# Performance work log

Measured on AMD Instinct MI355X. Metric: run time of the kernel, lower is better.

Reference implementation:

```python
import jax, jax.numpy as jnp
import numpy as np

S, N, LAT, HID, NH, NLAYERS = 8, 128, 128, 384, 8, 6
HT, WT, DT = 128, 128, 128
DIN, DOUT, RAD, LEVELS, FED = 1169, 3 + 3 * 128, 3, 4, 64


def sincos1d(d, pos):
    # MAE-style 1d sincos embedding, d even -> [..., d]
    omega = 1.0 / (10000.0 ** (jnp.arange(d // 2, dtype=jnp.float32) / (d / 2.0)))
    ang = pos[..., None] * omega
    return jnp.concatenate([jnp.sin(ang), jnp.cos(ang)], axis=-1)


def flow_embed(f, Cd=FED):
    # get_3d_embedding(flows, 64, cat_coords=True) -> [..., 3*Cd+3] = 195
    div = jnp.arange(0, Cd, 2, dtype=jnp.float32) * (1000.0 / Cd)
    outs = []
    for a in range(3):
        ang = f[..., a, None] * div
        pe = jnp.stack([jnp.sin(ang), jnp.cos(ang)], axis=-1).reshape(f.shape[:-1] + (Cd,))
        outs.append(pe)
    return jnp.concatenate(outs + [f], axis=-1)


def avg_pool2(x):
    B, Sv, Cc, H, W = x.shape
    return x.reshape(B, Sv, Cc, H // 2, 2, W // 2, 2).mean(axis=(4, 6))


def pyramid(fm):
    pyr = [fm]
    for _ in range(LEVELS - 1):
        fm = avg_pool2(fm)
        pyr.append(fm)
    return pyr


def bilinear_sample(corr, xy):
    # corr: [B,S,N,H,W]; xy: [B,S,N,P,2] pixel coords (x indexes W, y indexes H); zero padding
    B, Sv, Nn, H, W = corr.shape
    cf = corr.reshape(B, Sv, Nn, H * W)
    x, y = xy[..., 0], xy[..., 1]
    x0f = jnp.floor(x); y0f = jnp.floor(y)
    wx, wy = x - x0f, y - y0f
    x0 = x0f.astype(jnp.int32); y0 = y0f.astype(jnp.int32)

    def gather(xi, yi):
        ok = ((xi >= 0) & (xi < W) & (yi >= 0) & (yi < H)).astype(cf.dtype)
        idx = jnp.clip(yi, 0, H - 1) * W + jnp.clip(xi, 0, W - 1)
        v = jnp.take_along_axis(cf, idx.reshape(B, Sv, Nn, -1), axis=-1).reshape(idx.shape)
        return v * ok

    v00 = gather(x0, y0); v01 = gather(x0 + 1, y0)
    v10 = gather(x0, y0 + 1); v11 = gather(x0 + 1, y0 + 1)
    return v00 * (1 - wx) * (1 - wy) + v01 * wx * (1 - wy) + v10 * (1 - wx) * wy + v11 * wx * wy


def corr_sample(pyr, targets, coords):
    # RAFT/CoTracker CorrBlock: per-level dense correlation then (2r+1)^2 window bilinear lookup
    d = jnp.arange(-RAD, RAD + 1, dtype=jnp.float32)
    delta = jnp.stack(jnp.meshgrid(d, d, indexing="ij"), axis=-1).reshape(-1, 2)  # [49,2]
    scale = 1.0 / jnp.sqrt(jnp.float32(targets.shape[-1]))
    outs = []
    for l, fm in enumerate(pyr):
        corr = jnp.einsum("bsnc,bschw->bsnhw", targets, fm) * scale
        xy = coords[..., None, :] / (2.0 ** l) + delta
        outs.append(bilinear_sample(corr, xy))
    return jnp.concatenate(outs, axis=-1)  # [B,S,N,196]


def layernorm(x, g, b):
    m = x.mean(-1, keepdims=True)
    v = x.var(-1, keepdims=True)
    return (x - m) / jnp.sqrt(v + 1e-5) * g + b


def attention(x, Wqkv, bq, Wo, bo):
    M, T, H = x.shape
    dh = H // NH
    qkv = (x @ Wqkv + bq).reshape(M, T, 3, NH, dh)
    q, k, v = qkv[:, :, 0], qkv[:, :, 1], qkv[:, :, 2]
    att = jax.nn.softmax(jnp.einsum("mthd,mshd->mhts", q, k) / jnp.sqrt(jnp.float32(dh)), axis=-1)
    o = jnp.einsum("mhts,mshd->mthd", att, v).reshape(M, T, H)
    return o @ Wo + bo


def updateformer(x, support, W_in, b_in, lnp, Wqkv, bqkv, Wo, bo, W1, b1, W2, b2, W_out, b_out, Ws, bs):
    # x: [B,N,T,DIN]; alternating time (over T) and space (over N) pre-LN transformer blocks
    B, Np, T, _ = x.shape
    sproj = support @ Ws + bs  # [100,HID]
    h = x @ W_in + b_in + sproj.mean(axis=0)
    for i in range(NLAYERS):
        g1, bb1, g2, bb2 = lnp[i, 0], lnp[i, 1], lnp[i, 2], lnp[i, 3]
        if i % 2 == 0:
            y = h.reshape(B * Np, T, HID)
        else:
            y = h.transpose(0, 2, 1, 3).reshape(B * T, Np, HID)
        y = y + attention(layernorm(y, g1, bb1), Wqkv[i], bqkv[i], Wo[i], bo[i])
        z = layernorm(y, g2, bb2)
        y = y + jax.nn.gelu(z @ W1[i] + b1[i], approximate=False) @ W2[i] + b2[i]
        if i % 2 == 0:
            h = y.reshape(B, Np, T, HID)
        else:
            h = y.reshape(B, T, Np, HID).transpose(0, 2, 1, 3)
    return h @ W_out + b_out, sproj[None]


def groupnorm1(x, g, b):
    m = x.mean(-1, keepdims=True)
    v = x.var(-1, keepdims=True)
    return (x - m) / jnp.sqrt(v + 1e-5) * g + b


def _forward(fmapXY, fmapYZ, fmapXZ, coords_init, vis_init, track_mask, feat_init, support_features,
             W_in, b_in, lnp, Wqkv, bqkv, Wo, bo, W1, b1, W2, b2, W_out, b_out, Ws, bs,
             gn_g, gn_b, Wu, bu, Wvis, bvis, iters):
    B, Sv, Cc, H, W = fmapXY.shape
    D = fmapXZ.shape[-2]
    Nn = coords_init.shape[2]
    coords = coords_init
    ffeats = [feat_init[..., k] for k in range(3)]
    pyrXY, pyrYZ, pyrXZ = pyramid(fmapXY), pyramid(fmapYZ), pyramid(fmapXZ)
    grid_size = jnp.array([H, W, D], dtype=jnp.float32)
    # 3d sincos pos embed from query coords; 1169 padded to 1170 -> 390/axis, truncated back
    g = (coords[:, 0] / grid_size * 2.0 - 1.0) * 128.0  # [B,N,3]
    pe = jnp.concatenate([sincos1d(390, g[..., i]) for i in range(3)], axis=-1)[..., :DIN]
    pos_embed = pe.reshape(B * Nn, 1, DIN)
    times_embed = sincos1d(1170, jnp.arange(Sv, dtype=jnp.float32))[None, :, :DIN]
    support = support_features
    for _ in range(iters):
        coords = jax.lax.stop_gradient(coords)  # matches coords.detach()
        fxy = corr_sample(pyrXY, ffeats[0], coords[..., :2])
        fyz = corr_sample(pyrYZ, ffeats[1], coords[..., 1:3])
        fxz = corr_sample(pyrXZ, ffeats[2], coords[..., 0::2])
        fcorrs = jnp.concatenate([fxy, fyz, fxz], axis=-1)  # [B,S,N,588]
        fcorrs_ = fcorrs.transpose(0, 2, 1, 3).reshape(B * Nn, Sv, -1)
        flows_ = (coords - coords[:, :1]).transpose(0, 2, 1, 3).reshape(B * Nn, Sv, 3)
        flows_cat = flow_embed(flows_)  # [BN,S,195]
        ff = [f.transpose(0, 2, 1, 3).reshape(B * Nn, Sv, LAT) for f in ffeats]
        ffeats_ = jnp.concatenate(ff, axis=-1)  # [BN,S,384]
        # replicate torch's cat(dim=2)+permute+reshape layout exactly
        tmv = jnp.concatenate([track_mask, vis_init], axis=2).transpose(0, 2, 1, 3).reshape(B * Nn, Sv, 2)
        tin = jnp.concatenate([flows_cat, fcorrs_, ffeats_, tmv], axis=-1)  # [BN,S,1169]
        x = (tin + pos_embed + times_embed).reshape(B, Nn, Sv, DIN)
        delta, dse3 = updateformer(x, support, W_in, b_in, lnp, Wqkv, bqkv, Wo, bo, W1, b1, W2, b2, W_out, b_out, Ws, bs)
        support = support + dse3[0] / 100.0
        delta = delta.reshape(B * Nn, Sv, DOUT)
        d_coord = delta[..., :3].reshape(B, Nn, Sv, 3).transpose(0, 2, 1, 3)
        coords = coords + d_coord
        new_ffeats = []
        for k in range(3):
            dfk = delta[..., 3 + k * LAT:3 + (k + 1) * LAT]
            upd = jax.nn.gelu(groupnorm1(dfk, gn_g[k], gn_b[k]) @ Wu[k] + bu[k], approximate=False)
            new_ffeats.append(ffeats[k] + upd.reshape(B, Nn, Sv, LAT).transpose(0, 2, 1, 3))
        ffeats = new_ffeats
    vis = (jnp.concatenate(ffeats, axis=-1) @ Wvis + bvis)[..., 0]  # [B,S,N]
    return jnp.concatenate([coords, vis[..., None]], axis=-1)  # [B,S,N,4]


def setup_inputs() -> dict:
    key = jax.random.key(0)
    ks = jax.random.split(key, 16)
    f32 = jnp.float32
    B = 1
    fmapXY = jax.random.normal(ks[0], (B, S, LAT, HT, WT), f32)
    fmapYZ = jax.random.normal(ks[1], (B, S, LAT, DT, HT), f32)
    fmapXZ = jax.random.normal(ks[2], (B, S, LAT, DT, WT), f32)
    coords_init = jax.random.uniform(ks[3], (B, S, N, 3), f32) * 112.0 + 8.0
    vis_init = jnp.ones((B, S, N, 1), f32)
    track_mask = jnp.ones((B, S, N, 1), f32)
    feat_init = jax.random.normal(ks[4], (B, S, N, LAT, 3), f32)
    support_features = jnp.zeros((100, HID), f32) + 0.1
    w = lambda k, sh: jax.random.normal(k, sh, f32) * 0.02
    ln1 = jnp.stack([jnp.ones(HID, f32), jnp.zeros(HID, f32), jnp.ones(HID, f32), jnp.zeros(HID, f32)])
    params = dict(
        W_in=w(ks[5], (DIN, HID)), b_in=jnp.zeros((HID,), f32),
        lnp=jnp.tile(ln1[None], (NLAYERS, 1, 1)),
        Wqkv=w(ks[6], (NLAYERS, HID, 3 * HID)), bqkv=jnp.zeros((NLAYERS, 3 * HID), f32),
        Wo=w(ks[7], (NLAYERS, HID, HID)), bo=jnp.zeros((NLAYERS, HID), f32),
        W1=w(ks[8], (NLAYERS, HID, 4 * HID)), b1=jnp.zeros((NLAYERS, 4 * HID), f32),
        W2=w(ks[9], (NLAYERS, 4 * HID, HID)), b2=jnp.zeros((NLAYERS, HID), f32),
        W_out=w(ks[10], (HID, DOUT)), b_out=jnp.zeros((DOUT,), f32),
        Ws=w(ks[11], (HID, HID)), bs=jnp.zeros((HID,), f32),
        gn_g=jnp.ones((3, LAT), f32), gn_b=jnp.zeros((3, LAT), f32),
        Wu=w(ks[12], (3, LAT, LAT)), bu=jnp.zeros((3, LAT), f32),
        Wvis=w(ks[13], (3 * LAT, 1)), bvis=jnp.zeros((1,), f32),
    )
    return dict(fmapXY=fmapXY, fmapYZ=fmapYZ, fmapXZ=fmapXZ, coords_init=coords_init,
                vis_init=vis_init, track_mask=track_mask, feat_init=feat_init,
                support_features=support_features, iters=2, **params)


def reference(fmapXY, fmapYZ, fmapXZ, coords_init, vis_init, track_mask, feat_init, support_features,
              W_in, b_in, lnp, Wqkv, bqkv, Wo, bo, W1, b1, W2, b2, W_out, b_out, Ws, bs,
              gn_g, gn_b, Wu, bu, Wvis, bvis, iters):
    return _forward(fmapXY, fmapYZ, fmapXZ, coords_init, vis_init, track_mask, feat_init, support_features,
                    W_in, b_in, lnp, Wqkv, bqkv, Wo, bo, W1, b1, W2, b2, W_out, b_out, Ws, bs,
                    gn_g, gn_b, Wu, bu, Wvis, bvis, iters)
```

## Files before the change

kernel.cpp:

```cpp
#include <hip/hip_runtime.h>
#include <hip/hip_bf16.h>


#define DEVFN __device__ __forceinline__

typedef __attribute__((ext_vector_type(8))) short short8;
typedef __attribute__((ext_vector_type(4))) float f32x4;

static constexpr float INV_SQRT_DH = 0.14433756729740643f;
static constexpr float CORR_SCALE  = 0.08838834764831845f;
static constexpr size_t VSTRIDE = 22282240;

DEVFN float gelu_exact(float x){
  return 0.5f * x * (1.0f + erff(x * 0.7071067811865476f));
}
DEVFN short bf16_of(float f){
  __hip_bfloat16 b = __float2bfloat16(f);
  return *reinterpret_cast<short*>(&b);
}
DEVFN float bfu(uint32_t u16){ return __uint_as_float(u16 << 16); }
DEVFN float bf2f(__hip_bfloat16 b){ return __bfloat162float(b); }

DEVFN f32x4 MFMA(short8 a, short8 b, f32x4 c){
  return __builtin_amdgcn_mfma_f32_16x16x32_bf16(a,b,c,0,0,0);
}

template<int K, int MODE, bool AF32, int DEPTH>
static __device__ void mgemm_body(int bx, int by, const void* __restrict__ A, int lda,
                                  const __hip_bfloat16* __restrict__ Bt,
                                  float* __restrict__ C, int ldc,
                                  int M, int N, const float* __restrict__ bias, int tid){
  constexpr int NSTEP = K/32;
  int lane = tid & 63, wid = tid >> 6;
  int wr = wid >> 1, wc = wid & 1;
  int lr = lane & 15, lk = lane >> 4;
  int m0 = by*64 + wr*32;
  int n0 = bx*64 + wc*32;

  const __hip_bfloat16* Ab = (const __hip_bfloat16*)A;
  const float* Af = (const float*)A;
  size_t arow0 = (size_t)(m0 + lr)      * lda;
  size_t arow1 = (size_t)(m0 + 16 + lr) * lda;
  size_t brow0 = (size_t)(n0 + lr)      * K;
  size_t brow1 = (size_t)(n0 + 16 + lr) * K;

  auto loadA = [&](size_t ro, int k0)->short8{
    if constexpr (AF32){
      const float* p = Af + ro + k0 + lk*8;
      short8 r;
      #pragma unroll
      for (int j=0;j<8;j++) r[j] = bf16_of(p[j]);
      return r;
    } else {
      return *reinterpret_cast<const short8*>(Ab + ro + k0 + lk*8);
    }
  };
  auto loadB = [&](size_t ro, int k0)->short8{
    return *reinterpret_cast<const short8*>(Bt + ro + k0 + lk*8);
  };

  short8 a0[DEPTH], a1[DEPTH], b0[DEPTH], b1[DEPTH];
  #pragma unroll
  for (int p=0;p<DEPTH;p++){
    if (p < NSTEP){
      a0[p]=loadA(arow0,p*32); a1[p]=loadA(arow1,p*32);
      b0[p]=loadB(brow0,p*32); b1[p]=loadB(brow1,p*32);
    }
  }
  f32x4 acc00 = {}, acc01 = {}, acc10 = {}, acc11 = {};
  #pragma unroll
  for (int t=0;t<NSTEP;t++){
    const int cur = t % DEPTH;
    acc00 = MFMA(a0[cur],b0[cur],acc00);
    acc01 = MFMA(a0[cur],b1[cur],acc01);
    acc10 = MFMA(a1[cur],b0[cur],acc10);
    acc11 = MFMA(a1[cur],b1[cur],acc11);
    if (t+DEPTH < NSTEP){
      int k0 = (t+DEPTH)*32;
      a0[cur]=loadA(arow0,k0); a1[cur]=loadA(arow1,k0);
      b0[cur]=loadB(brow0,k0); b1[cur]=loadB(brow1,k0);
    }
  }

  f32x4 accs[2][2] = {{acc00, acc01},{acc10, acc11}};
  #pragma unroll
  for (int mi=0;mi<2;mi++){
    #pragma unroll
    for (int ni=0;ni<2;ni++){
      int c = n0 + ni*16 + lr;
      if (c >= N) continue;
      float bv = bias ? bias[c] : 0.0f;
      #pragma unroll
      for (int reg=0;reg<4;reg++){
        int r = m0 + mi*16 + lk*4 + reg;
        if (r >= M) continue;
        float v = accs[mi][ni][reg] + bv;
        if (MODE==0) C[(size_t)r*ldc + c] = v;
        else C[(size_t)r*ldc + c] += v;
      }
    }
  }
}

__global__ void transpose_init_k(const float* __restrict__ inXY, const float* __restrict__ inYZ,
                                 const float* __restrict__ inXZ, __hip_bfloat16* __restrict__ pyr,
                                 float* coords, const float* cinit,
                                 float* ff, const float* feat_init,
                                 float* support, const float* sfeat,
                                 float* posE, float* timE){
  int bid = blockIdx.x;
  int tid = threadIdx.x;
  if (bid >= 12288){
    int idx = (bid - 12288)*256 + tid;
    if (idx < 3072)  coords[idx]  = cinit[idx];
    if (idx < 49152){
      int row = idx / 384;
      support[idx] = (row < 100) ? sfeat[idx] : 0.0f;
    }
    if (idx < 393216){
      int k = idx / 131072, rest = idx % 131072;
      ff[idx] = feat_init[(size_t)rest*3 + k];
    }
    if (idx < 149632){
      int n = idx / 1169, d = idx % 1169;
      int i = d / 390, dd = d % 390;
      float c = cinit[n*3 + i];
      float g = (c / 128.0f * 2.0f - 1.0f) * 128.0f;
      int m = (dd < 195) ? dd : dd - 195;
      float om = powf(10000.0f, -(float)m / 195.0f);
      float ang = g * om;
      posE[idx] = (dd < 195) ? sinf(ang) : cosf(ang);
    }
    if (idx < 9352){
      int s = idx / 1169, d = idx % 1169;
      int m = (d < 585) ? d : d - 585;
      float om = powf(10000.0f, -(float)m / 585.0f);
      float ang = (float)s * om;
      timE[idx] = (d < 585) ? sinf(ang) : cosf(ang);
    }
    return;
  }
  __shared__ float tile[128][33];
  int vz = bid >> 9;
  int v = vz >> 3, s = vz & 7;
  const float* in = (v==0) ? inXY : ((v==1) ? inYZ : inXZ);
  int h0 = (bid & 511) * 32;
  const float* ib = in + (size_t)s*128*16384;
  int chunk = tid & 7;
  int cbase = tid >> 3;
  #pragma unroll
  for (int r=0;r<4;r++){
    int c = cbase + r*32;
    float4 f = *reinterpret_cast<const float4*>(ib + (size_t)c*16384 + h0 + chunk*4);
    tile[c][chunk*4+0]=f.x; tile[c][chunk*4+1]=f.y;
    tile[c][chunk*4+2]=f.z; tile[c][chunk*4+3]=f.w;
  }
  __syncthreads();
  __hip_bfloat16* ob = pyr + (size_t)v*VSTRIDE + (size_t)s*16384*128;
  int w = tid >> 6, lane = tid & 63;
  #pragma unroll
  for (int rr=0;rr<8;rr++){
    int hw = w*8 + rr;
    uint32_t lo = (uint32_t)(uint16_t)bf16_of(tile[2*lane][hw]);
    uint32_t hi = (uint32_t)(uint16_t)bf16_of(tile[2*lane+1][hw]);
    reinterpret_cast<uint32_t*>(ob + (size_t)(h0+hw)*128)[lane] = lo | (hi<<16);
  }
}

__global__ void pool2_k(__hip_bfloat16* __restrict__ pyr, size_t in_off, size_t out_off, int So){
  int idx = blockIdx.x*256 + threadIdx.x;
  int total = 8*So*So*128;
  if (idx >= total) return;
  const __hip_bfloat16* in = pyr + (size_t)blockIdx.z*VSTRIDE + in_off;
  __hip_bfloat16* out      = pyr + (size_t)blockIdx.z*VSTRIDE + out_off;
  int c = idx & 127;
  int x = (idx >> 7) % So;
  int y = ((idx >> 7) / So) % So;
  int s = idx / (So*So*128);
  int Si = So*2;
  const __hip_bfloat16* b0 = in + (((size_t)s*Si + 2*y)*Si + 2*x)*128 + c;
  float v = bf2f(b0[0]) + bf2f(b0[128])
          + bf2f(b0[(size_t)Si*128]) + bf2f(b0[(size_t)Si*128 + 128]);
  out[idx] = __float2bfloat16(v*0.25f);
}

__global__ void wtrans_all_k(const float* Ws, const float* W_in, const float* Wqkv,
                             const float* Wo, const float* W1, const float* W2,
                             const float* W_out, const float* Wu,
                             __hip_bfloat16* WsT, __hip_bfloat16* WinT, __hip_bfloat16* WqkvT,
                             __hip_bfloat16* WoT, __hip_bfloat16* W1T, __hip_bfloat16* W2T,
                             __hip_bfloat16* WoutT, __hip_bfloat16* WuT){
  __shared__ float tile[32][33];
  int z = blockIdx.z;
  const float* in; __hip_bfloat16* out; int K,N,Kp,Np;
  if (z==0){ in=Ws; out=WsT; K=384;N=384;Kp=384;Np=384; }
  else if (z==1){ in=W_in; out=WinT; K=1169;N=384;Kp=1184;Np=384; }
  else if (z<8){ int l=z-2; in=Wqkv+(size_t)l*442368; out=WqkvT+(size_t)l*442368; K=384;N=1152;Kp=384;Np=1152; }
  else if (z<14){ int l=z-8; in=Wo+(size_t)l*147456; out=WoT+(size_t)l*147456; K=384;N=384;Kp=384;Np=384; }
  else if (z<20){ int l=z-14; in=W1+(size_t)l*589824; out=W1T+(size_t)l*589824; K=384;N=1536;Kp=384;Np=1536; }
  else if (z<26){ int l=z-20; in=W2+(size_t)l*589824; out=W2T+(size_t)l*589824; K=1536;N=384;Kp=1536;Np=384; }
  else if (z==26){ in=W_out; out=WoutT; K=384;N=387;Kp=384;Np=448; }
  else { int l=z-27; in=Wu+(size_t)l*16384; out=WuT+(size_t)l*16384; K=128;N=128;Kp=128;Np=128; }
  int MK = (K>Kp)?K:Kp, MN = (N>Np)?N:Np;
  int kb = blockIdx.y*32, nb = blockIdx.x*32;
  if (kb >= MK || nb >= MN) return;
  int tx = threadIdx.x & 31, ty = threadIdx.x >> 5;
  #pragma unroll
  for (int r=0;r<4;r++){
    int k = kb + ty + r*8, n = nb + tx;
    tile[ty+r*8][tx] = (k < K && n < N) ? in[(size_t)k*N + n] : 0.0f;
  }
  __syncthreads();
  #pragma unroll
  for (int r=0;r<4;r++){
    int n = nb + ty + r*8, k = kb + tx;
    if (n < Np && k < Kp) out[(size_t)n*Kp + k] = __float2bfloat16(tile[tx][ty+r*8]);
  }
}

__global__ void assemble_x_k(__hip_bfloat16* __restrict__ xbuf, const float* __restrict__ posE,
                             const float* __restrict__ timE, const float* __restrict__ coords,
                             const float* __restrict__ ff, const float* __restrict__ tmask,
                             const float* __restrict__ vinit,
                             const float* __restrict__ support,
                             const __hip_bfloat16* __restrict__ WsT,
                             float* __restrict__ sproj, const float* __restrict__ bs){
  if (blockIdx.x >= 1024){
    int b = blockIdx.x - 1024;
    mgemm_body<384,0,true,3>(b%6, b/6, support,384, WsT, sproj,384, 100,384, bs, threadIdx.x);
    return;
  }
  int r = blockIdx.x;
  int n = r >> 3, s = r & 7;
  for (int d = threadIdx.x; d < 1184; d += blockDim.x){
    __hip_bfloat16* dst = xbuf + (size_t)r*1184 + d;
    if (d >= 1169){ *dst = __float2bfloat16(0.0f); continue; }
    float base = posE[(size_t)n*1169 + d] + timE[(size_t)s*1169 + d];
    if (d >= 195 && d < 783){ *dst = __float2bfloat16(base); continue; }
    float val;
    if (d < 195){
      if (d >= 192){
        int a = d - 192;
        val = coords[(s*128+n)*3 + a] - coords[n*3 + a];
      } else {
        int a = d >> 6, dd = d & 63;
        float f = coords[(s*128+n)*3 + a] - coords[n*3 + a];
        float ang = f * (31.25f * (float)(dd >> 1));
        val = (dd & 1) ? cosf(ang) : sinf(ang);
      }
    } else if (d < 1167){
      int cidx = d - 783, k = cidx >> 7, cc = cidx & 127;
      val = ff[(size_t)k*131072 + (size_t)(s*128+n)*128 + cc];
    } else {
      int c = d - 1167;
      int flat = n*16 + s*2 + c;
      int n2 = flat >> 3, s2 = flat & 7;
      val = (n2 < 128) ? tmask[s2*128 + n2] : vinit[s2*128 + (n2-128)];
    }
    *dst = __float2bfloat16(val + base);
  }
}

__global__ void corr_k(const __hip_bfloat16* __restrict__ pyr, const float* __restrict__ coords,
                       const float* __restrict__ ff, __hip_bfloat16* __restrict__ xbuf,
                       const float* __restrict__ sproj, const float* __restrict__ b_in,
                       float* __restrict__ bias2, float* __restrict__ support){
  if (blockIdx.x >= 3072){
    int idx = (blockIdx.x - 3072)*256 + threadIdx.x;
    if (idx < 38400) support[idx] += sproj[idx]*0.01f;
    else if (idx < 38784){
      int c = idx - 38400;
      float s = 0.0f;
      for (int r=0;r<100;r++) s += sproj[r*384 + c];
      bias2[c] = b_in[c] + s*0.01f;
    }
    return;
  }
  __shared__ float t[128];
  __shared__ float p[4][64];
  int bid = blockIdx.x;
  int view = bid >> 10, s = (bid >> 7) & 7, n = bid & 127;
  int tid = threadIdx.x;
  int l = tid >> 6, t64 = tid & 63;
  if (tid < 128) t[tid] = ff[(size_t)view*131072 + (size_t)(s*128+n)*128 + tid];
  int ax = (view==1) ? 1 : 0;
  int ay = (view==0) ? 1 : 2;
  float X = coords[(s*128+n)*3 + ax];
  float Y = coords[(s*128+n)*3 + ay];
  const __hip_bfloat16* vb = pyr + (size_t)view*VSTRIDE;
  __syncthreads();

  int sz = 128 >> l;
  size_t loff = (l==0) ? 0ull : (l==1 ? 16777216ull : (l==2 ? 20971520ull : 22020096ull));
  float inv = 1.0f / (float)(1 << l);
  float cx = X * inv, cy = Y * inv;
  float x0f = floorf(cx), y0f = floorf(cy);
  float wx = cx - x0f, wy = cy - y0f;
  int ix0 = (int)x0f, iy0 = (int)y0f;
  int px = ix0 - 3 + (t64 & 7);
  int py = iy0 - 3 + (t64 >> 3);
  float acc = 0.0f;
  if (px >= 0 && px < sz && py >= 0 && py < sz){
    const uint2* row = reinterpret_cast<const uint2*>(vb + loff + (((size_t)s*sz + py)*sz + px)*128);
    #pragma unroll
    for (int c4=0;c4<32;c4++){
      uint2 u = row[c4];
      float f0 = __uint_as_float(u.x << 16);
      float f1 = __uint_as_float(u.x & 0xffff0000u);
      float f2 = __uint_as_float(u.y << 16);
      float f3 = __uint_as_float(u.y & 0xffff0000u);
      acc += t[c4*4+0]*f0 + t[c4*4+1]*f1 + t[c4*4+2]*f2 + t[c4*4+3]*f3;
    }
  }
  p[l][t64] = acc;
  __syncthreads();
  if (t64 < 49){
    int i = t64 / 7, jj = t64 % 7;
    float v = p[l][jj*8+i]       * (1.0f-wx)*(1.0f-wy)
            + p[l][jj*8+i+1]     * wx*(1.0f-wy)
            + p[l][(jj+1)*8+i]   * (1.0f-wx)*wy
            + p[l][(jj+1)*8+i+1] * wx*wy;
    __hip_bfloat16* dst = xbuf + (size_t)(n*8+s)*1184 + 195 + view*196 + l*49 + t64;
    *dst = __float2bfloat16(__bfloat162float(*dst) + v * CORR_SCALE);
  }
}

template<int K, int MODE, bool AF32, int DEPTH>
__global__ __launch_bounds__(256) void mgemm_k(const void* __restrict__ A, int lda,
                                               const __hip_bfloat16* __restrict__ Bt,
                                               float* __restrict__ C, int ldc,
                                               int M, int N,
                                               const float* __restrict__ bias){
  mgemm_body<K,MODE,AF32,DEPTH>(blockIdx.x, blockIdx.y, A, lda, Bt, C, ldc, M, N, bias, threadIdx.x);
}

__global__ __launch_bounds__(256) void ln_qkv_k(const float* __restrict__ A,
                                                const float* __restrict__ gamma,
                                                const float* __restrict__ beta,
                                                const __hip_bfloat16* __restrict__ Bt,
                                                __hip_bfloat16* __restrict__ Cbf,
                                                const float* __restrict__ bias){
  constexpr int LDSS = 392;
  __shared__ short Asm[64*LDSS];
  int tid = threadIdx.x, lane = tid & 63, w = tid >> 6;
  int m0 = blockIdx.y*64, n0b = blockIdx.x*128;

  float gg[6], bb[6];
  #pragma unroll
  for (int e=0;e<6;e++){ gg[e] = gamma[lane+e*64]; bb[e] = beta[lane+e*64]; }
  for (int rr=0; rr<16; rr++){
    int r = w*16 + rr;
    const float* row = A + (size_t)(m0+r)*384;
    float x[6]; float sum = 0.0f;
    #pragma unroll
    for (int e=0;e<6;e++){ x[e] = row[lane+e*64]; sum += x[e]; }
    #pragma unroll
    for (int o=32;o>0;o>>=1) sum += __shfl_xor(sum, o);
    float mean = sum * (1.0f/384.0f);
    float vs = 0.0f;
    #pragma unroll
    for (int e=0;e<6;e++){ float d = x[e]-mean; vs += d*d; }
    #pragma unroll
    for (int o=32;o>0;o>>=1) vs += __shfl_xor(vs, o);
    float invstd = 1.0f / sqrtf(vs*(1.0f/384.0f) + 1e-5f);
    #pragma unroll
    for (int e=0;e<6;e++)
      Asm[r*LDSS + lane + e*64] = bf16_of((x[e]-mean)*invstd*gg[e] + bb[e]);
  }
  __syncthreads();

  int wr = w >> 1, wc = w & 1;
  int lr = lane & 15, lk = lane >> 4;
  const __hip_bfloat16* Brow[4];
  #pragma unroll
  for (int ni=0;ni<4;ni++) Brow[ni] = Bt + (size_t)(n0b + wc*64 + ni*16 + lr)*384;

  short8 bfrag[4][4];
  #pragma unroll
  for (int p=0;p<4;p++)
    #pragma unroll
    for (int ni=0;ni<4;ni++)
      bfrag[p][ni] = *(const short8*)(Brow[ni] + p*32 + lk*8);

  f32x4 acc[2][4] = {};
  #pragma unroll
  for (int t=0;t<12;t++){
    const int cur = t & 3;
    short8 a0 = *(const short8*)(&Asm[(wr*32+lr)*LDSS    + t*32 + lk*8]);
    short8 a1 = *(const short8*)(&Asm[(wr*32+16+lr)*LDSS + t*32 + lk*8]);
    #pragma unroll
    for (int ni=0;ni<4;ni++){
      acc[0][ni] = MFMA(a0,bfrag[cur][ni],acc[0][ni]);
      acc[1][ni] = MFMA(a1,bfrag[cur][ni],acc[1][ni]);
    }
    if (t+4 < 12){
      #pragma unroll
      for (int ni=0;ni<4;ni++)
        bfrag[cur][ni] = *(const short8*)(Brow[ni] + (t+4)*32 + lk*8);
    }
  }
  #pragma unroll
  for (int mi=0;mi<2;mi++){
    #pragma unroll
    for (int ni=0;ni<4;ni++){
      int c = n0b + wc*64 + ni*16 + lr;
      float bv = bias[c];
      #pragma unroll
      for (int reg=0;reg<4;reg++){
        int r = m0 + wr*32 + mi*16 + lk*4 + reg;
        Cbf[(size_t)r*1152 + c] = __float2bfloat16(acc[mi][ni][reg] + bv);
      }
    }
  }
}

template<bool GELU>
__global__ __launch_bounds__(256) void lngemm_k(const float* __restrict__ A,
                                                const float* __restrict__ gamma,
                                                const float* __restrict__ beta,
                                                const __hip_bfloat16* __restrict__ Bt,
                                                __hip_bfloat16* __restrict__ Cbf, int ldc,
                                                const float* __restrict__ bias){
  constexpr int LDSS = 392;
  __shared__ short Asm[64*LDSS];
  int tid = threadIdx.x, lane = tid & 63, w = tid >> 6;
  int m0 = blockIdx.y*64, n0b = blockIdx.x*128;

  float gg[6], bb[6];
  #pragma unroll
  for (int e=0;e<6;e++){ gg[e] = gamma[lane+e*64]; bb[e] = beta[lane+e*64]; }
  for (int rr=0; rr<16; rr++){
    int r = w*16 + rr;
    const float* row = A + (size_t)(m0+r)*384;
    float x[6]; float sum = 0.0f;
    #pragma unroll
    for (int e=0;e<6;e++){ x[e] = row[lane+e*64]; sum += x[e]; }
    #pragma unroll
    for (int o=32;o>0;o>>=1) sum += __shfl_xor(sum, o);
    float mean = sum * (1.0f/384.0f);
    float vs = 0.0f;
    #pragma unroll
    for (int e=0;e<6;e++){ float d = x[e]-mean; vs += d*d; }
    #pragma unroll
    for (int o=32;o>0;o>>=1) vs += __shfl_xor(vs, o);
    float invstd = 1.0f / sqrtf(vs*(1.0f/384.0f) + 1e-5f);
    #pragma unroll
    for (int e=0;e<6;e++)
      Asm[r*LDSS + lane + e*64] = bf16_of((x[e]-mean)*invstd*gg[e] + bb[e]);
  }
  __syncthreads();

  int wr = w >> 1, wc = w & 1;
  int lr = lane & 15, lk = lane >> 4;
  const __hip_bfloat16* Brow[4];
  #pragma unroll
  for (int ni=0;ni<4;ni++) Brow[ni] = Bt + (size_t)(n0b + wc*64 + ni*16 + lr)*384;

  short8 bfrag[2][4];
  #pragma unroll
  for (int p=0;p<2;p++)
    #pragma unroll
    for (int ni=0;ni<4;ni++)
      bfrag[p][ni] = *(const short8*)(Brow[ni] + p*32 + lk*8);

  f32x4 acc[2][4] = {};
  #pragma unroll
  for (int t=0;t<12;t++){
    const int cur = t & 1;
    short8 a0 = *(const short8*)(&Asm[(wr*32+lr)*LDSS    + t*32 + lk*8]);
    short8 a1 = *(const short8*)(&Asm[(wr*32+16+lr)*LDSS + t*32 + lk*8]);
    #pragma unroll
    for (int ni=0;ni<4;ni++){
      acc[0][ni] = MFMA(a0,bfrag[cur][ni],acc[0][ni]);
      acc[1][ni] = MFMA(a1,bfrag[cur][ni],acc[1][ni]);
    }
    if (t+2 < 12){
      #pragma unroll
      for (int ni=0;ni<4;ni++)
        bfrag[cur][ni] = *(const short8*)(Brow[ni] + (t+2)*32 + lk*8);
    }
  }
  #pragma unroll
  for (int mi=0;mi<2;mi++){
    #pragma unroll
    for (int ni=0;ni<4;ni++){
      int c = n0b + wc*64 + ni*16 + lr;
      float bv = bias[c];
      #pragma unroll
      for (int reg=0;reg<4;reg++){
        int r = m0 + wr*32 + mi*16 + lk*4 + reg;
        float v = acc[mi][ni][reg] + bv;
        Cbf[(size_t)r*ldc + c] = __float2bfloat16(GELU ? gelu_exact(v) : v);
      }
    }
  }
}

__global__ __launch_bounds__(256) void gn_wu_k(const float* __restrict__ dbuf,
                                               const float* __restrict__ gn_g,
                                               const float* __restrict__ gn_b,
                                               const __hip_bfloat16* __restrict__ WuT,
                                               const float* __restrict__ bu,
                                               float* __restrict__ ff,
                                               float* __restrict__ coords){
  __shared__ short Asm[64*136];
  int z = blockIdx.z, by = blockIdx.y, bx = blockIdx.x;
  int tid = threadIdx.x, lane = tid & 63, w = tid >> 6;
  const float* g = gn_g + z*128;
  const float* b = gn_b + z*128;

  for (int rr=0; rr<16; ++rr){
    int r = w*16 + rr;
    const float* row = dbuf + (size_t)(by*64 + r)*387 + 3 + z*128;
    float x0 = row[lane], x1 = row[lane+64];
    float sum = x0 + x1;
    #pragma unroll
    for (int o=32;o>0;o>>=1) sum += __shfl_xor(sum, o);
    float mean = sum * (1.0f/128.0f);
    float d0 = x0-mean, d1 = x1-mean;
    float vs = d0*d0 + d1*d1;
    #pragma unroll
    for (int o=32;o>0;o>>=1) vs += __shfl_xor(vs, o);
    float invstd = 1.0f / sqrtf(vs*(1.0f/128.0f) + 1e-5f);
    Asm[r*136 + lane]      = bf16_of(d0*invstd*g[lane] + b[lane]);
    Asm[r*136 + lane + 64] = bf16_of(d1*invstd*g[lane+64] + b[lane+64]);
  }
  if (z == 0 && bx == 0 && by < 12){
    int idx = by*256 + tid;
    if (idx < 3072){
      int a = idx % 3, sn = idx / 3;
      int ss = sn >> 7, nn = sn & 127;
      coords[idx] += dbuf[(size_t)(nn*8+ss)*387 + a];
    }
  }
  __syncthreads();

  int wr = w >> 1, wc = w & 1;
  int lr = lane & 15, lk = lane >> 4;
  int m0l = wr*32;
  int n0 = bx*64 + wc*32;
  const __hip_bfloat16* Bt = WuT + (size_t)z*16384;
  const float* bias = bu + (size_t)z*128;
  float* aux = ff + (size_t)z*131072;
  f32x4 acc00={}, acc01={}, acc10={}, acc11={};
  #pragma unroll
  for (int t=0;t<4;t++){
    short8 a0 = *(const short8*)(&Asm[(m0l+lr)*136    + t*32 + lk*8]);
    short8 a1 = *(const short8*)(&Asm[(m0l+16+lr)*136 + t*32 + lk*8]);
    short8 b0 = *(const short8*)(Bt + (size_t)(n0+lr)*128    + t*32 + lk*8);
    short8 b1 = *(const short8*)(Bt + (size_t)(n0+16+lr)*128 + t*32 + lk*8);
    acc00 = MFMA(a0,b0,acc00);
    acc01 = MFMA(a0,b1,acc01);
    acc10 = MFMA(a1,b0,acc10);
    acc11 = MFMA(a1,b1,acc11);
  }
  f32x4 accs[2][2] = {{acc00, acc01},{acc10, acc11}};
  #pragma unroll
  for (int mi=0;mi<2;mi++){
    #pragma unroll
    for (int ni=0;ni<2;ni++){
      int c = n0 + ni*16 + lr;
      float bv = bias[c];
      #pragma unroll
      for (int reg=0;reg<4;reg++){
        int r = by*64 + m0l + mi*16 + lk*4 + reg;
        float v = accs[mi][ni][reg] + bv;
        int ss = r & 7, nn2 = r >> 3;
        aux[((size_t)(ss*128+nn2))*128 + c] += gelu_exact(v);
      }
    }
  }
}

__global__ __launch_bounds__(512) void attn_even_k(const __hip_bfloat16* __restrict__ qkv,
                                                   __hip_bfloat16* __restrict__ attout){
  int g = blockIdx.x;
  int h = threadIdx.x >> 6;
  int lane = threadIdx.x & 63;
  int t = lane >> 3, j = lane & 7;
  const short* qs = (const short*)qkv;

  float q[48], kk[48];
  {
    const short8* qp = (const short8*)(qs + (size_t)(g*8+t)*1152 + h*48);
    const short8* kp = (const short8*)(qs + (size_t)(g*8+j)*1152 + 384 + h*48);
    #pragma unroll
    for (int c=0;c<6;c++){
      short8 qv = qp[c], kv = kp[c];
      #pragma unroll
      for (int e=0;e<8;e++){
        q[c*8+e]  = bfu((uint16_t)qv[e]);
        kk[c*8+e] = bfu((uint16_t)kv[e]);
      }
    }
  }
  float s = 0.0f;
  #pragma unroll
  for (int d=0;d<48;d++) s += q[d]*kk[d];
  s *= INV_SQRT_DH;
  float mx = s;
  #pragma unroll
  for (int o=1;o<8;o<<=1) mx = fmaxf(mx, __shfl_xor(mx, o));
  float e = expf(s - mx);
  float l = e;
  #pragma unroll
  for (int o=1;o<8;o<<=1) l += __shfl_xor(l, o);
  float p = e / l;

  float o6[6] = {0,0,0,0,0,0};
  #pragma unroll
  for (int jp=0;jp<8;jp++){
    float pj = __shfl(p, (lane & 56) | jp);
    const uint32_t* vp = (const uint32_t*)(qs + (size_t)(g*8+jp)*1152 + 768 + h*48 + j*6);
    uint32_t w0 = vp[0], w1 = vp[1], w2 = vp[2];
    o6[0] += pj * bfu(w0 & 0xffffu); o6[1] += pj * bfu(w0 >> 16);
    o6[2] += pj * bfu(w1 & 0xffffu); o6[3] += pj * bfu(w1 >> 16);
    o6[4] += pj * bfu(w2 & 0xffffu); o6[5] += pj * bfu(w2 >> 16);
  }
  uint32_t r0 = ((uint32_t)(uint16_t)bf16_of(o6[1]) << 16) | (uint16_t)bf16_of(o6[0]);
  uint32_t r1 = ((uint32_t)(uint16_t)bf16_of(o6[3]) << 16) | (uint16_t)bf16_of(o6[2]);
  uint32_t r2 = ((uint32_t)(uint16_t)bf16_of(o6[5]) << 16) | (uint16_t)bf16_of(o6[4]);
  uint32_t* op = (uint32_t*)((short*)attout + (size_t)(g*8+t)*384 + h*48 + j*6);
  op[0] = r0; op[1] = r1; op[2] = r2;
}

__global__ __launch_bounds__(256) void attn_odd_mfma_k(const __hip_bfloat16* __restrict__ qkv,
                                                       __hip_bfloat16* __restrict__ attout){
  __shared__ char smem[47872];
  short* Qb = (short*)smem;
  short* Kb = (short*)(smem + 18432);
  short* Pb = (short*)smem;
  short* Vt = (short*)(smem + 34816);
  int g = blockIdx.x & 7, h = blockIdx.x >> 3;
  int tid = threadIdx.x;

  const short* qs = (const short*)qkv;
  for (int idx = tid; idx < 768; idx += 256){
    int t = idx / 6, dblk = idx % 6;
    size_t base = (size_t)(t*8+g)*1152 + h*48 + dblk*8;
    *(short8*)(Qb + t*72 + dblk*8) = *(const short8*)(qs + base);
    *(short8*)(Kb + t*72 + dblk*8) = *(const short8*)(qs + base + 384);
  }
  short8 zz = {};
  for (int idx = tid; idx < 384; idx += 256){
    int t = idx / 3, dblk = idx % 3;
    *(short8*)(Qb + t*72 + 48 + dblk*8) = zz;
    *(short8*)(Kb + t*72 + 48 + dblk*8) = zz;
  }
  __syncthreads();

  int lane = tid & 63, w = tid >> 6;
  int lr = lane & 15, lk = lane >> 4;
  int m0 = w*32;

  f32x4 S[2][8] = {};
  #pragma unroll
  for (int ks=0; ks<2; ks++){
    short8 a0 = *(const short8*)(Qb + (m0+lr)*72    + ks*32 + lk*8);
    short8 a1 = *(const short8*)(Qb + (m0+16+lr)*72 + ks*32 + lk*8);
    #pragma unroll
    for (int ni=0; ni<8; ni++){
      short8 b = *(const short8*)(Kb + (ni*16+lr)*72 + ks*32 + lk*8);
      S[0][ni] = MFMA(a0,b,S[0][ni]);
      S[1][ni] = MFMA(a1,b,S[1][ni]);
    }
  }

  #pragma unroll
  for (int mi=0;mi<2;mi++){
    #pragma unroll
    for (int reg=0;reg<4;reg++){
      float m = -1e30f;
      #pragma unroll
      for (int ni=0;ni<8;ni++) m = fmaxf(m, S[mi][ni][reg]);
      #pragma unroll
      for (int o=1;o<16;o<<=1) m = fmaxf(m, __shfl_xor(m, o));
      m *= INV_SQRT_DH;
      float l = 0.0f;
      #pragma unroll
      for (int ni=0;ni<8;ni++){
        float p = expf(S[mi][ni][reg]*INV_SQRT_DH - m);
        S[mi][ni][reg] = p;
        l += p;
      }
      #pragma unroll
      for (int o=1;o<16;o<<=1) l += __shfl_xor(l, o);
      float inv = 1.0f/l;
      #pragma unroll
      for (int ni=0;ni<8;ni++) S[mi][ni][reg] *= inv;
    }
  }
  __syncthreads();

  for (int idx = tid; idx < 768; idx += 256){
    int j = idx / 6, dblk = idx % 6;
    short8 v = *(const short8*)(qs + (size_t)(j*8+g)*1152 + 768 + h*48 + dblk*8);
    #pragma unroll
    for (int e=0;e<8;e++) Vt[(dblk*8+e)*136 + j] = v[e];
  }
  #pragma unroll
  for (int mi=0;mi<2;mi++)
    #pragma unroll
    for (int ni=0;ni<8;ni++)
      #pragma unroll
      for (int reg=0;reg<4;reg++)
        Pb[(m0+mi*16+lk*4+reg)*136 + ni*16+lr] = bf16_of(S[mi][ni][reg]);
  __syncthreads();

  f32x4 O[2][3] = {};
  #pragma unroll
  for (int ks=0; ks<4; ks++){
    short8 a0 = *(const short8*)(Pb + (m0+lr)*136    + ks*32 + lk*8);
    short8 a1 = *(const short8*)(Pb + (m0+16+lr)*136 + ks*32 + lk*8);
    #pragma unroll
    for (int ni=0; ni<3; ni++){
      short8 b = *(const short8*)(Vt + (ni*16+lr)*136 + ks*32 + lk*8);
      O[0][ni] = MFMA(a0,b,O[0][ni]);
      O[1][ni] = MFMA(a1,b,O[1][ni]);
    }
  }
  #pragma unroll
  for (int mi=0;mi<2;mi++){
    #pragma unroll
    for (int ni=0;ni<3;ni++){
      #pragma unroll
      for (int reg=0;reg<4;reg++){
        int q = m0 + mi*16 + lk*4 + reg;
        int d = ni*16 + lr;
        attout[(size_t)(q*8+g)*384 + h*48 + d] = __float2bfloat16(O[mi][ni][reg]);
      }
    }
  }
}

__global__ void final_out_k(const float* __restrict__ coords, const float* __restrict__ ff,
                            const float* __restrict__ Wvis, const float* __restrict__ bvis,
                            float* __restrict__ out){
  int sn = blockIdx.x*64 + threadIdx.x;
  if (sn >= 1024) return;
  float acc = bvis[0];
  for (int k=0;k<3;k++)
    for (int c=0;c<128;c++)
      acc += ff[(size_t)k*131072 + (size_t)sn*128 + c] * Wvis[k*128 + c];
  out[sn*4+0] = coords[sn*3+0];
  out[sn*4+1] = coords[sn*3+1];
  out[sn*4+2] = coords[sn*3+2];
  out[sn*4+3] = acc;
}


extern "C" void kernel_launch(void* const* d_in, const int* in_sizes, int n_in,
                              void* d_out, int out_size, void* d_ws, size_t ws_size,
                              hipStream_t stream) {
  const float* fmapXY   = (const float*)d_in[0];
  const float* fmapYZ   = (const float*)d_in[1];
  const float* fmapXZ   = (const float*)d_in[2];
  const float* cinit    = (const float*)d_in[3];
  const float* vinit    = (const float*)d_in[4];
  const float* tmask    = (const float*)d_in[5];
  const float* feat_init= (const float*)d_in[6];
  const float* sfeat    = (const float*)d_in[7];
  const float* W_in     = (const float*)d_in[9];
  const float* b_in     = (const float*)d_in[10];
  const float* lnp      = (const float*)d_in[11];
  const float* Wqkv     = (const float*)d_in[12];
  const float* bqkv     = (const float*)d_in[13];
  const float* Wo       = (const float*)d_in[14];
  const float* bo       = (const float*)d_in[15];
  const float* W1       = (const float*)d_in[16];
  const float* b1       = (const float*)d_in[17];
  const float* W2       = (const float*)d_in[18];
  const float* b2       = (const float*)d_in[19];
  const float* W_out    = (const float*)d_in[20];
  const float* b_out    = (const float*)d_in[21];
  const float* Ws       = (const float*)d_in[22];
  const float* bs       = (const float*)d_in[23];
  const float* gn_g     = (const float*)d_in[24];
  const float* gn_b     = (const float*)d_in[25];
  const float* Wu       = (const float*)d_in[26];
  const float* bu       = (const float*)d_in[27];
  const float* Wvis     = (const float*)d_in[28];
  const float* bvis     = (const float*)d_in[29];
  const int ITERS = 2;

  char* wp = (char*)d_ws;
  auto alloc = [&](size_t bytes)->char* {
    char* p = wp; wp += (bytes + 255) & ~(size_t)255; return p;
  };
  __hip_bfloat16* pyr = (__hip_bfloat16*)alloc(3ull*VSTRIDE*2);
  float* coords = (float*)alloc(3072ull*4);
  float* ff     = (float*)alloc(393216ull*4);
  float* support= (float*)alloc(49152ull*4);
  float* sproj  = (float*)alloc(38400ull*4);
  float* bias2  = (float*)alloc(384ull*4);
  float* posE   = (float*)alloc(149632ull*4);
  float* timE   = (float*)alloc(9352ull*4);
  float* hbuf   = (float*)alloc(393216ull*4);
  float* dbuf   = (float*)alloc(396288ull*4);
  __hip_bfloat16* xbuf_bf = (__hip_bfloat16*)alloc(1212416ull*2);
  __hip_bfloat16* qkv_bf  = (__hip_bfloat16*)alloc(1179648ull*2);
  __hip_bfloat16* atto_bf = (__hip_bfloat16*)alloc(393216ull*2);
  __hip_bfloat16* ffb_bf  = (__hip_bfloat16*)alloc(1572864ull*2);
  __hip_bfloat16* WsT   = (__hip_bfloat16*)alloc(147456ull*2);
  __hip_bfloat16* WinT  = (__hip_bfloat16*)alloc(454656ull*2);
  __hip_bfloat16* WqkvT = (__hip_bfloat16*)alloc(2654208ull*2);
  __hip_bfloat16* WoT   = (__hip_bfloat16*)alloc(884736ull*2);
  __hip_bfloat16* W1T   = (__hip_bfloat16*)alloc(3538944ull*2);
  __hip_bfloat16* W2T   = (__hip_bfloat16*)alloc(3538944ull*2);
  __hip_bfloat16* WoutT = (__hip_bfloat16*)alloc(172032ull*2);
  __hip_bfloat16* WuT   = (__hip_bfloat16*)alloc(49152ull*2);
  if ((size_t)(wp - (char*)d_ws) > ws_size) return;

  transpose_init_k<<<13824, 256, 0, stream>>>(fmapXY, fmapYZ, fmapXZ, pyr,
                                              coords, cinit, ff, feat_init,
                                              support, sfeat, posE, timE);
  pool2_k<<<dim3((8*64*64*128 + 255)/256,1,3), 256, 0, stream>>>(pyr, 0,        16777216, 64);
  pool2_k<<<dim3((8*32*32*128 + 255)/256,1,3), 256, 0, stream>>>(pyr, 16777216, 20971520, 32);
  pool2_k<<<dim3((8*16*16*128 + 255)/256,1,3), 256, 0, stream>>>(pyr, 20971520, 22020096, 16);
  wtrans_all_k<<<dim3(48,48,30), 256, 0, stream>>>(Ws, W_in, Wqkv, Wo, W1, W2, W_out, Wu,
                                                   WsT, WinT, WqkvT, WoT, W1T, W2T, WoutT, WuT);

  for (int it=0; it<ITERS; ++it){
    assemble_x_k<<<1036, 256, 0, stream>>>(xbuf_bf, posE, timE, coords, ff, tmask, vinit,
                                           support, WsT, sproj, bs);
    corr_k<<<3224, 256, 0, stream>>>(pyr, coords, ff, xbuf_bf, sproj, b_in, bias2, support);

    mgemm_k<1184,0,false,6><<<dim3(6,16), 256, 0, stream>>>(xbuf_bf,1184, WinT, hbuf,384, 1024,384, bias2);

    for (int i=0;i<6;i++){
      const float* g1  = lnp + (size_t)(i*4+0)*384;
      const float* bb1 = lnp + (size_t)(i*4+1)*384;
      const float* g2  = lnp + (size_t)(i*4+2)*384;
      const float* bb2 = lnp + (size_t)(i*4+3)*384;

      ln_qkv_k<<<dim3(9,16), 256, 0, stream>>>(hbuf, g1, bb1, WqkvT + (size_t)i*442368,
                                               qkv_bf, bqkv + i*1152);
      if ((i & 1) == 0) attn_even_k<<<128, 512, 0, stream>>>(qkv_bf, atto_bf);
      else              attn_odd_mfma_k<<<64, 256, 0, stream>>>(qkv_bf, atto_bf);
      mgemm_k<384,1,false,3><<<dim3(6,16), 256, 0, stream>>>(atto_bf,384, WoT + (size_t)i*147456,
                                                             hbuf,384, 1024,384, bo + i*384);
      lngemm_k<true><<<dim3(12,16), 256, 0, stream>>>(hbuf, g2, bb2, W1T + (size_t)i*589824,
                                                      ffb_bf, 1536, b1 + i*1536);
      mgemm_k<1536,1,false,6><<<dim3(6,16), 256, 0, stream>>>(ffb_bf,1536, W2T + (size_t)i*589824,
                                                              hbuf,384, 1024,384, b2 + i*384);
    }

    mgemm_k<384,0,true,3><<<dim3(7,16), 256, 0, stream>>>(hbuf,384, WoutT, dbuf,387, 1024,387, b_out);
    gn_wu_k<<<dim3(2,16,3), 256, 0, stream>>>(dbuf, gn_g, gn_b, WuT, bu, ff, coords);
  }

  final_out_k<<<16, 64, 0, stream>>>(coords, ff, Wvis, bvis, (float*)d_out);
}
```

Baseline: 1.455 ms.

## Split GEMMs into single-wave blocks and narrow LN-GEMM column tiles

The plain GEMMs now launch as one-wavefront blocks, each computing a 32x32 tile, so 384 blocks replace 96 four-wave blocks and the small M=1024 problems spread across more of the GPU's compute units. The LN+QKV and LN+FFN1 kernels are merged into one templated lngemm with 64-column tiles instead of 128, which doubles the grid. The B-prefetch depth becomes a template parameter. The cost is that the layer norm is recomputed by twice as many blocks, and each block does less work to amortize launch and its loads.

```diff
diff --git a/kernel.cpp b/kernel.cpp
--- a/kernel.cpp
+++ b/kernel.cpp
@@ -26,16 +26,12 @@
 }
 
 template<int K, int MODE, bool AF32, int DEPTH>
-static __device__ void mgemm_body(int bx, int by, const void* __restrict__ A, int lda,
+static __device__ void wgemm_body(int m0, int n0, const void* __restrict__ A, int lda,
                                   const __hip_bfloat16* __restrict__ Bt,
                                   float* __restrict__ C, int ldc,
-                                  int M, int N, const float* __restrict__ bias, int tid){
+                                  int M, int N, const float* __restrict__ bias, int lane){
   constexpr int NSTEP = K/32;
-  int lane = tid & 63, wid = tid >> 6;
-  int wr = wid >> 1, wc = wid & 1;
   int lr = lane & 15, lk = lane >> 4;
-  int m0 = by*64 + wr*32;
-  int n0 = bx*64 + wc*32;
 
   const __hip_bfloat16* Ab = (const __hip_bfloat16*)A;
   const float* Af = (const float*)A;
@@ -100,6 +96,27 @@
       }
     }
   }
+}
+
+template<int K, int MODE, bool AF32, int DEPTH>
+__global__ __launch_bounds__(64) void wgemm_k(const void* __restrict__ A, int lda,
+                                              const __hip_bfloat16* __restrict__ Bt,
+                                              float* __restrict__ C, int ldc,
+                                              int M, int N,
+                                              const float* __restrict__ bias){
+  wgemm_body<K,MODE,AF32,DEPTH>(blockIdx.y*32, blockIdx.x*32, A, lda, Bt, C, ldc,
+                                M, N, bias, threadIdx.x & 63);
+}
+
+template<int K, int MODE, bool AF32, int DEPTH>
+static __device__ void mgemm_body(int bx, int by, const void* __restrict__ A, int lda,
+                                  const __hip_bfloat16* __restrict__ Bt,
+                                  float* __restrict__ C, int ldc,
+                                  int M, int N, const float* __restrict__ bias, int tid){
+  int wid = tid >> 6;
+  int wr = wid >> 1, wc = wid & 1;
+  wgemm_body<K,MODE,AF32,DEPTH>(by*64 + wr*32, bx*64 + wc*32, A, lda, Bt, C, ldc,
+                                M, N, bias, tid & 63);
 }
 
 __global__ void transpose_init_k(const float* __restrict__ inXY, const float* __restrict__ inYZ,
@@ -325,96 +342,7 @@
   }
 }
 
-template<int K, int MODE, bool AF32, int DEPTH>
-__global__ __launch_bounds__(256) void mgemm_k(const void* __restrict__ A, int lda,
-                                               const __hip_bfloat16* __restrict__ Bt,
-                                               float* __restrict__ C, int ldc,
-                                               int M, int N,
-                                               const float* __restrict__ bias){
-  mgemm_body<K,MODE,AF32,DEPTH>(blockIdx.x, blockIdx.y, A, lda, Bt, C, ldc, M, N, bias, threadIdx.x);
-}
-
-__global__ __launch_bounds__(256) void ln_qkv_k(const float* __restrict__ A,
-                                                const float* __restrict__ gamma,
-                                                const float* __restrict__ beta,
-                                                const __hip_bfloat16* __restrict__ Bt,
-                                                __hip_bfloat16* __restrict__ Cbf,
-                                                const float* __restrict__ bias){
-  constexpr int LDSS = 392;
-  __shared__ short Asm[64*LDSS];
-  int tid = threadIdx.x, lane = tid & 63, w = tid >> 6;
-  int m0 = blockIdx.y*64, n0b = blockIdx.x*128;
-
-  float gg[6], bb[6];
-  #pragma unroll
-  for (int e=0;e<6;e++){ gg[e] = gamma[lane+e*64]; bb[e] = beta[lane+e*64]; }
-  for (int rr=0; rr<16; rr++){
-    int r = w*16 + rr;
-    const float* row = A + (size_t)(m0+r)*384;
-    float x[6]; float sum = 0.0f;
-    #pragma unroll
-    for (int e=0;e<6;e++){ x[e] = row[lane+e*64]; sum += x[e]; }
-    #pragma unroll
-    for (int o=32;o>0;o>>=1) sum += __shfl_xor(sum, o);
-    float mean = sum * (1.0f/384.0f);
-    float vs = 0.0f;
-    #pragma unroll
-    for (int e=0;e<6;e++){ float d = x[e]-mean; vs += d*d; }
-    #pragma unroll
-    for (int o=32;o>0;o>>=1) vs += __shfl_xor(vs, o);
-    float invstd = 1.0f / sqrtf(vs*(1.0f/384.0f) + 1e-5f);
-    #pragma unroll
-    for (int e=0;e<6;e++)
-      Asm[r*LDSS + lane + e*64] = bf16_of((x[e]-mean)*invstd*gg[e] + bb[e]);
-  }
-  __syncthreads();
-
-  int wr = w >> 1, wc = w & 1;
-  int lr = lane & 15, lk = lane >> 4;
-  const __hip_bfloat16* Brow[4];
-  #pragma unroll
-  for (int ni=0;ni<4;ni++) Brow[ni] = Bt + (size_t)(n0b + wc*64 + ni*16 + lr)*384;
-
-  short8 bfrag[4][4];
-  #pragma unroll
-  for (int p=0;p<4;p++)
-    #pragma unroll
-    for (int ni=0;ni<4;ni++)
-      bfrag[p][ni] = *(const short8*)(Brow[ni] + p*32 + lk*8);
-
-  f32x4 acc[2][4] = {};
-  #pragma unroll
-  for (int t=0;t<12;t++){
-    const int cur = t & 3;
-    short8 a0 = *(const short8*)(&Asm[(wr*32+lr)*LDSS    + t*32 + lk*8]);
-    short8 a1 = *(const short8*)(&Asm[(wr*32+16+lr)*LDSS + t*32 + lk*8]);
-    #pragma unroll
-    for (int ni=0;ni<4;ni++){
-      acc[0][ni] = MFMA(a0,bfrag[cur][ni],acc[0][ni]);
-      acc[1][ni] = MFMA(a1,bfrag[cur][ni],acc[1][ni]);
-    }
-    if (t+4 < 12){
-      #pragma unroll
-      for (int ni=0;ni<4;ni++)
-        bfrag[cur][ni] = *(const short8*)(Brow[ni] + (t+4)*32 + lk*8);
-    }
-  }
-  #pragma unroll
-  for (int mi=0;mi<2;mi++){
-    #pragma unroll
-    for (int ni=0;ni<4;ni++){
-      int c = n0b + wc*64 + ni*16 + lr;
-      float bv = bias[c];
-      #pragma unroll
-      for (int reg=0;reg<4;reg++){
-        int r = m0 + wr*32 + mi*16 + lk*4 + reg;
-        Cbf[(size_t)r*1152 + c] = __float2bfloat16(acc[mi][ni][reg] + bv);
-      }
-    }
-  }
-}
-
-template<bool GELU>
+template<bool GELU, int BDEPTH>
 __global__ __launch_bounds__(256) void lngemm_k(const float* __restrict__ A,
                                                 const float* __restrict__ gamma,
                                                 const float* __restrict__ beta,
@@ -424,7 +352,7 @@
   constexpr int LDSS = 392;
   __shared__ short Asm[64*LDSS];
   int tid = threadIdx.x, lane = tid & 63, w = tid >> 6;
-  int m0 = blockIdx.y*64, n0b = blockIdx.x*128;
+  int m0 = blockIdx.y*64, n0b = blockIdx.x*64;
 
   float gg[6], bb[6];
   #pragma unroll
@@ -452,44 +380,41 @@
 
   int wr = w >> 1, wc = w & 1;
   int lr = lane & 15, lk = lane >> 4;
-  const __hip_bfloat16* Brow[4];
-  #pragma unroll
-  for (int ni=0;ni<4;ni++) Brow[ni] = Bt + (size_t)(n0b + wc*64 + ni*16 + lr)*384;
-
-  short8 bfrag[2][4];
-  #pragma unroll
-  for (int p=0;p<2;p++)
-    #pragma unroll
-    for (int ni=0;ni<4;ni++)
-      bfrag[p][ni] = *(const short8*)(Brow[ni] + p*32 + lk*8);
-
-  f32x4 acc[2][4] = {};
+  const __hip_bfloat16* Brow0 = Bt + (size_t)(n0b + wc*32 + lr)*384;
+  const __hip_bfloat16* Brow1 = Brow0 + 16*384;
+
+  short8 b0[BDEPTH], b1[BDEPTH];
+  #pragma unroll
+  for (int p=0;p<BDEPTH;p++){
+    b0[p] = *(const short8*)(Brow0 + p*32 + lk*8);
+    b1[p] = *(const short8*)(Brow1 + p*32 + lk*8);
+  }
+  f32x4 acc00={}, acc01={}, acc10={}, acc11={};
   #pragma unroll
   for (int t=0;t<12;t++){
-    const int cur = t & 1;
+    const int cur = t % BDEPTH;
     short8 a0 = *(const short8*)(&Asm[(wr*32+lr)*LDSS    + t*32 + lk*8]);
     short8 a1 = *(const short8*)(&Asm[(wr*32+16+lr)*LDSS + t*32 + lk*8]);
-    #pragma unroll
-    for (int ni=0;ni<4;ni++){
-      acc[0][ni] = MFMA(a0,bfrag[cur][ni],acc[0][ni]);
-      acc[1][ni] = MFMA(a1,bfrag[cur][ni],acc[1][ni]);
-    }
-    if (t+2 < 12){
-      #pragma unroll
-      for (int ni=0;ni<4;ni++)
-        bfrag[cur][ni] = *(const short8*)(Brow[ni] + (t+2)*32 + lk*8);
-    }
-  }
+    acc00 = MFMA(a0,b0[cur],acc00);
+    acc01 = MFMA(a0,b1[cur],acc01);
+    acc10 = MFMA(a1,b0[cur],acc10);
+    acc11 = MFMA(a1,b1[cur],acc11);
+    if (t+BDEPTH < 12){
+      b0[cur] = *(const short8*)(Brow0 + (t+BDEPTH)*32 + lk*8);
+      b1[cur] = *(const short8*)(Brow1 + (t+BDEPTH)*32 + lk*8);
+    }
+  }
+  f32x4 accs[2][2] = {{acc00, acc01},{acc10, acc11}};
   #pragma unroll
   for (int mi=0;mi<2;mi++){
     #pragma unroll
-    for (int ni=0;ni<4;ni++){
-      int c = n0b + wc*64 + ni*16 + lr;
+    for (int ni=0;ni<2;ni++){
+      int c = n0b + wc*32 + ni*16 + lr;
       float bv = bias[c];
       #pragma unroll
       for (int reg=0;reg<4;reg++){
         int r = m0 + wr*32 + mi*16 + lk*4 + reg;
-        float v = acc[mi][ni][reg] + bv;
+        float v = accs[mi][ni][reg] + bv;
         Cbf[(size_t)r*ldc + c] = __float2bfloat16(GELU ? gelu_exact(v) : v);
       }
     }
@@ -825,7 +750,7 @@
                                            support, WsT, sproj, bs);
     corr_k<<<3224, 256, 0, stream>>>(pyr, coords, ff, xbuf_bf, sproj, b_in, bias2, support);
 
-    mgemm_k<1184,0,false,6><<<dim3(6,16), 256, 0, stream>>>(xbuf_bf,1184, WinT, hbuf,384, 1024,384, bias2);
+    wgemm_k<1184,0,false,6><<<dim3(12,32), 64, 0, stream>>>(xbuf_bf,1184, WinT, hbuf,384, 1024,384, bias2);
 
     for (int i=0;i<6;i++){
       const float* g1  = lnp + (size_t)(i*4+0)*384;
@@ -833,19 +758,19 @@
       const float* g2  = lnp + (size_t)(i*4+2)*384;
       const float* bb2 = lnp + (size_t)(i*4+3)*384;
 
-      ln_qkv_k<<<dim3(9,16), 256, 0, stream>>>(hbuf, g1, bb1, WqkvT + (size_t)i*442368,
-                                               qkv_bf, bqkv + i*1152);
+      lngemm_k<false,4><<<dim3(18,16), 256, 0, stream>>>(hbuf, g1, bb1, WqkvT + (size_t)i*442368,
+                                                         qkv_bf, 1152, bqkv + i*1152);
       if ((i & 1) == 0) attn_even_k<<<128, 512, 0, stream>>>(qkv_bf, atto_bf);
       else              attn_odd_mfma_k<<<64, 256, 0, stream>>>(qkv_bf, atto_bf);
-      mgemm_k<384,1,false,3><<<dim3(6,16), 256, 0, stream>>>(atto_bf,384, WoT + (size_t)i*147456,
+      wgemm_k<384,1,false,3><<<dim3(12,32), 64, 0, stream>>>(atto_bf,384, WoT + (size_t)i*147456,
                                                              hbuf,384, 1024,384, bo + i*384);
-      lngemm_k<true><<<dim3(12,16), 256, 0, stream>>>(hbuf, g2, bb2, W1T + (size_t)i*589824,
-                                                      ffb_bf, 1536, b1 + i*1536);
-      mgemm_k<1536,1,false,6><<<dim3(6,16), 256, 0, stream>>>(ffb_bf,1536, W2T + (size_t)i*589824,
+      lngemm_k<true,2><<<dim3(24,16), 256, 0, stream>>>(hbuf, g2, bb2, W1T + (size_t)i*589824,
+                                                        ffb_bf, 1536, b1 + i*1536);
+      wgemm_k<1536,1,false,6><<<dim3(12,32), 64, 0, stream>>>(ffb_bf,1536, W2T + (size_t)i*589824,
                                                               hbuf,384, 1024,384, b2 + i*384);
     }
 
-    mgemm_k<384,0,true,3><<<dim3(7,16), 256, 0, stream>>>(hbuf,384, WoutT, dbuf,387, 1024,387, b_out);
+    wgemm_k<384,0,true,3><<<dim3(13,32), 64, 0, stream>>>(hbuf,384, WoutT, dbuf,387, 1024,387, b_out);
     gn_wu_k<<<dim3(2,16,3), 256, 0, stream>>>(dbuf, gn_g, gn_b, WuT, bu, ff, coords);
   }
 
```

Measured after the change: 1.306 ms. 10.2% less time.
